# Performance work log

Measured on AMD Instinct MI355X. Metric: run time of the kernel, lower is better.

The kernel has to match this reference:

```python
import jax, jax.numpy as jnp
import numpy as np

HIDDEN = 1024
INTER = 4096
NUM_EXPERTS = 8
TOP_K = 2
NUM_TOKENS = 8192


def setup_inputs() -> dict:
    key = jax.random.key(0)
    k_x, k_r, k_w1, k_w2 = jax.random.split(key, 4)
    x = jax.random.normal(k_x, (NUM_TOKENS, HIDDEN), dtype=jnp.float32)
    router_w = jax.random.normal(k_r, (NUM_EXPERTS, HIDDEN), dtype=jnp.float32) * 0.02
    expert_w1 = jax.random.normal(k_w1, (NUM_EXPERTS, HIDDEN, INTER), dtype=jnp.float32) * 0.02
    # torch init: std = 0.02 / sqrt(2 * num_experts)
    expert_w2 = jax.random.normal(k_w2, (NUM_EXPERTS, INTER, HIDDEN), dtype=jnp.float32) * (0.02 / (2 * NUM_EXPERTS) ** 0.5)
    return {"x": x, "router_w": router_w, "expert_w1": expert_w1, "expert_w2": expert_w2}


def reference(x, router_w, expert_w1, expert_w2):
    num_tokens = x.shape[0]
    # Router: logits -> softmax -> top-k -> renormalize (matches torch.topk on probs)
    router_logits = x @ router_w.T                      # [T, E]
    probs = jax.nn.softmax(router_logits, axis=-1)       # [T, E]
    top_vals, top_idx = jax.lax.top_k(probs, TOP_K)      # [T, K]
    top_vals = top_vals / jnp.sum(top_vals, axis=-1, keepdims=True)

    # Auxiliary load-balancing loss (uses only the top-1 expert, as in torch code)
    expert_mask = jax.nn.one_hot(top_idx[:, 0], NUM_EXPERTS, dtype=x.dtype)  # [T, E]
    tokens_per_expert = expert_mask.sum(axis=0)                              # [E]
    router_prob = probs.mean(axis=0)                                         # [E]
    aux_loss = jnp.sum(tokens_per_expert / num_tokens * router_prob) * NUM_EXPERTS

    # Per-token combine weight for each expert (scatter top-k weights to dense [T, E])
    combine = jnp.zeros((num_tokens, NUM_EXPERTS), dtype=x.dtype)
    combine = combine.at[jnp.arange(num_tokens)[:, None], top_idx].add(top_vals)

    # Per-expert 2-layer MLP (silu), weighted combine. Loop over fixed small E.
    output = jnp.zeros_like(x)
    for e in range(NUM_EXPERTS):
        h = jax.nn.silu(x @ expert_w1[e])            # [T, I]
        output = output + combine[:, e:e + 1] * (h @ expert_w2[e])
    return output, aux_loss
```

## Files before the change

### kernel.cpp

```cpp
#include <hip/hip_runtime.h>
#include <hip/hip_bf16.h>
#include <stdint.h>

#define NTOK  8192
#define HID   1024
#define INTER 4096
#define NEXP  8
#define NSLOT (NTOK * 2)

typedef __attribute__((ext_vector_type(4))) float f32x4;
typedef __attribute__((ext_vector_type(8))) short bf16x8;
typedef __attribute__((ext_vector_type(4))) short bf16x4;

__device__ __forceinline__ short f2bf(float f) {
  union { float f; uint32_t u; } v; v.f = f;
  uint32_t u = v.u;
  u += 0x7FFFu + ((u >> 16) & 1u);
  return (short)(u >> 16);
}

__device__ __forceinline__ void glds16(const short* g, short* l) {
  __builtin_amdgcn_global_load_lds(
      (const __attribute__((address_space(1))) void*)g,
      (__attribute__((address_space(3))) void*)l, 16, 0, 0);
}

__global__ __launch_bounds__(256) void castx_k(const float* __restrict__ in,
                                               short* __restrict__ out) {
  size_t i = ((size_t)blockIdx.x * 256 + threadIdx.x) * 4;
  f32x4 v = *(const f32x4*)(in + i);
  bf16x4 o = { f2bf(v.x), f2bf(v.y), f2bf(v.z), f2bf(v.w) };
  *(bf16x4*)(out + i) = o;
}

__global__ __launch_bounds__(256) void router_k(
    const float* __restrict__ x, const float* __restrict__ rw,
    int* __restrict__ top_idx, float* __restrict__ top_w,
    float* __restrict__ probsum, float* __restrict__ cnt1) {
  __shared__ float lrw[NEXP * HID];
  __shared__ float red[4][2 * NEXP];
  int tid = threadIdx.x;
  for (int i = tid * 4; i < NEXP * HID; i += 1024)
    *(f32x4*)(lrw + i) = *(const f32x4*)(rw + i);
  __syncthreads();
  int lane = tid & 63;
  int wv = tid >> 6;
  float pacc[NEXP], cacc[NEXP];
#pragma unroll
  for (int e = 0; e < NEXP; e++) { pacc[e] = 0.f; cacc[e] = 0.f; }
#pragma unroll
  for (int it = 0; it < 4; it++) {
    int t = blockIdx.x * 16 + it * 4 + wv;
    const float* xr = x + (size_t)t * HID;
    float acc[NEXP];
#pragma unroll
    for (int e = 0; e < NEXP; e++) acc[e] = 0.f;
#pragma unroll
    for (int k4 = 0; k4 < 4; k4++) {
      int k = k4 * 256 + lane * 4;
      f32x4 xv = *(const f32x4*)(xr + k);
#pragma unroll
      for (int e = 0; e < NEXP; e++) {
        f32x4 rv = *(const f32x4*)(lrw + e * HID + k);
        acc[e] += xv.x * rv.x + xv.y * rv.y + xv.z * rv.z + xv.w * rv.w;
      }
    }
#pragma unroll
    for (int e = 0; e < NEXP; e++) {
#pragma unroll
      for (int off = 32; off > 0; off >>= 1)
        acc[e] += __shfl_xor(acc[e], off);
    }
    float mx = acc[0];
#pragma unroll
    for (int e = 1; e < NEXP; e++) mx = fmaxf(mx, acc[e]);
    float p[NEXP], s = 0.f;
#pragma unroll
    for (int e = 0; e < NEXP; e++) { p[e] = expf(acc[e] - mx); s += p[e]; }
    float inv = 1.f / s;
    float p1 = -1.f, p2 = -1.f; int i1 = 0, i2 = 0;
#pragma unroll
    for (int e = 0; e < NEXP; e++) {
      float pe = p[e] * inv;
      p[e] = pe;
      if (pe > p1)      { p2 = p1; i2 = i1; p1 = pe; i1 = e; }
      else if (pe > p2) { p2 = pe; i2 = e; }
    }
    if (lane == 0) {
      float rs = 1.f / (p1 + p2);
      top_idx[t * 2] = i1; top_idx[t * 2 + 1] = i2;
      top_w[t * 2] = p1 * rs; top_w[t * 2 + 1] = p2 * rs;
#pragma unroll
      for (int e = 0; e < NEXP; e++) {
        pacc[e] += p[e];
        cacc[e] += (i1 == e) ? 1.f : 0.f;
      }
    }
  }
  if (lane == 0) {
#pragma unroll
    for (int e = 0; e < NEXP; e++) {
      red[wv][e] = pacc[e];
      red[wv][NEXP + e] = cacc[e];
    }
  }
  __syncthreads();
  if (tid < NEXP) {
    float s = 0.f, c = 0.f;
#pragma unroll
    for (int w = 0; w < 4; w++) { s += red[w][tid]; c += red[w][NEXP + tid]; }
    atomicAdd(&probsum[tid], s);
    atomicAdd(&cnt1[tid], c);
  }
}

__global__ void aux_k(const float* probsum, const float* cnt1, float* out_aux) {
  if (threadIdx.x == 0 && blockIdx.x == 0) {
    float s = 0.f;
    for (int e = 0; e < NEXP; e++) s += cnt1[e] * probsum[e];
    out_aux[0] = s * (float)NEXP / ((float)NTOK * (float)NTOK);
  }
}

__global__ void lists_k(const int* __restrict__ top_idx, int* __restrict__ cnt,
                        int* __restrict__ lists) {
  int i = blockIdx.x * 256 + threadIdx.x;
  if (i < NSLOT) {
    int e = top_idx[i];
    int pos = atomicAdd(cnt + e, 1);
    lists[e * NTOK + pos] = i;
  }
}

__global__ __launch_bounds__(256) void transpose_k(
    const float* __restrict__ in, short* __restrict__ out, int K, int N) {
  __shared__ short tile[64][72];
  int e = blockIdx.z;
  in  += (size_t)e * K * N;
  out += (size_t)e * K * N;
  int n0 = blockIdx.x * 64, k0 = blockIdx.y * 64;
  int tid = threadIdx.x;
#pragma unroll
  for (int i = 0; i < 4; i++) {
    int k = (tid >> 4) + i * 16;
    int c = (tid & 15) * 4;
    f32x4 v = *(const f32x4*)(in + (size_t)(k0 + k) * N + n0 + c);
    tile[k][c] = f2bf(v.x); tile[k][c + 1] = f2bf(v.y);
    tile[k][c + 2] = f2bf(v.z); tile[k][c + 3] = f2bf(v.w);
  }
  __syncthreads();
#pragma unroll
  for (int i = 0; i < 2; i++) {
    int cid = tid + i * 256;
    int n = cid >> 3, kk = (cid & 7) * 8;
    bf16x8 o;
#pragma unroll
    for (int j = 0; j < 8; j++) o[j] = tile[kk + j][n];
    *(bf16x8*)(out + (size_t)(n0 + n) * K + k0 + kk) = o;
  }
}

template <int KDIM, bool L1>
__global__ __launch_bounds__(256) void moe_gemm_k(
    const short* __restrict__ A, const short* __restrict__ Bt,
    void* __restrict__ outp, const int* __restrict__ cnt,
    const int* __restrict__ lists, const float* __restrict__ top_w, int Ndim) {
  int e = blockIdx.z;
  int ce = cnt[e];
  int m0 = blockIdx.y * 128;
  if (m0 >= ce) return;
  int n0 = blockIdx.x * 128;
  const int* list = lists + e * NTOK;
  const short* B = Bt + (size_t)e * Ndim * KDIM;

  __shared__ short As[128 * 32];
  __shared__ short Bs[128 * 32];
  __shared__ int   sSlot[128];
  __shared__ float sW[128];

  int tid = threadIdx.x;
  if (tid < 128) {
    int idx = m0 + tid;
    if (idx >= ce) idx = ce - 1;
    int slot = list[idx];
    sSlot[tid] = slot;
    sW[tid] = L1 ? 0.f : top_w[slot];
  }
  __syncthreads();

  int r1 = tid >> 2, cs = tid & 3;
  int r2 = r1 + 64;
  int q1 = (cs ^ ((r1 >> 1) & 3)) * 8;
  int q2 = (cs ^ ((r2 >> 1) & 3)) * 8;
  int ar1 = L1 ? (sSlot[r1] >> 1) : sSlot[r1];
  int ar2 = L1 ? (sSlot[r2] >> 1) : sSlot[r2];
  const short* gA1 = A + (size_t)ar1 * KDIM + q1;
  const short* gA2 = A + (size_t)ar2 * KDIM + q2;
  const short* gB1 = B + (size_t)(n0 + r1) * KDIM + q1;
  const short* gB2 = B + (size_t)(n0 + r2) * KDIM + q2;
  short* lA1 = As + tid * 8;
  short* lA2 = As + 2048 + tid * 8;
  short* lB1 = Bs + tid * 8;
  short* lB2 = Bs + 2048 + tid * 8;

  int lane = tid & 63, wave = tid >> 6;
  int wm = wave & 1, wn = wave >> 1;
  int lr = lane & 15, quad = lane >> 4;
  int aoff[4], boff[4];
#pragma unroll
  for (int mi = 0; mi < 4; mi++) {
    int r = wm * 64 + mi * 16 + lr;
    aoff[mi] = r * 32 + (quad ^ ((r >> 1) & 3)) * 8;
  }
#pragma unroll
  for (int ni = 0; ni < 4; ni++) {
    int n = wn * 64 + ni * 16 + lr;
    boff[ni] = n * 32 + (quad ^ ((n >> 1) & 3)) * 8;
  }

  f32x4 acc[4][4] = {};

  for (int kt = 0; kt < KDIM / 32; kt++) {
    int ko = kt * 32;
    glds16(gA1 + ko, lA1);
    glds16(gA2 + ko, lA2);
    glds16(gB1 + ko, lB1);
    glds16(gB2 + ko, lB2);
    __syncthreads();
    bf16x8 af[4], bfg[4];
#pragma unroll
    for (int mi = 0; mi < 4; mi++) af[mi] = *(const bf16x8*)(As + aoff[mi]);
#pragma unroll
    for (int ni = 0; ni < 4; ni++) bfg[ni] = *(const bf16x8*)(Bs + boff[ni]);
#pragma unroll
    for (int mi = 0; mi < 4; mi++)
#pragma unroll
      for (int ni = 0; ni < 4; ni++)
        acc[mi][ni] = __builtin_amdgcn_mfma_f32_16x16x32_bf16(af[mi], bfg[ni], acc[mi][ni], 0, 0, 0);
    __syncthreads();
  }

  int ncol0 = n0 + wn * 64 + lr;
#pragma unroll
  for (int mi = 0; mi < 4; mi++) {
#pragma unroll
    for (int rg = 0; rg < 4; rg++) {
      int r = wm * 64 + mi * 16 + quad * 4 + rg;
      int gm = m0 + r;
      if (gm < ce) {
        int slot = sSlot[r];
#pragma unroll
        for (int ni = 0; ni < 4; ni++) {
          float v = acc[mi][ni][rg];
          int col = ncol0 + ni * 16;
          if (L1) {
            float sv = v / (1.f + expf(-v));
            ((short*)outp)[(size_t)slot * Ndim + col] = f2bf(sv);
          } else {
            atomicAdd((float*)outp + (size_t)(slot >> 1) * Ndim + col, v * sW[r]);
          }
        }
      }
    }
  }
}

extern "C" void kernel_launch(void* const* d_in, const int* in_sizes, int n_in,
                              void* d_out, int out_size, void* d_ws, size_t ws_size,
                              hipStream_t stream) {
  const float* x  = (const float*)d_in[0];
  const float* rw = (const float*)d_in[1];
  const float* w1 = (const float*)d_in[2];
  const float* w2 = (const float*)d_in[3];
  float* out = (float*)d_out;

  char* ws = (char*)d_ws;
  size_t off = 0;
  auto alloc = [&](size_t b) { void* p = ws + off; off += (b + 255) & ~(size_t)255; return p; };
  short* wt    = (short*)alloc((size_t)NEXP * HID * INTER * 2);
  short* h     = (short*)alloc((size_t)NSLOT * INTER * 2);
  short* xb    = (short*)alloc((size_t)NTOK * HID * 2);
  int*   tidx  = (int*)alloc(NSLOT * 4);
  float* tw    = (float*)alloc(NSLOT * 4);
  int*   lists = (int*)alloc(NEXP * NTOK * 4);
  int*   cnt   = (int*)alloc(256);
  float* probsum = (float*)(cnt + 8);
  float* cnt1    = (float*)(cnt + 16);

  hipMemsetAsync(cnt, 0, 256, stream);
  hipMemsetAsync(out, 0, (size_t)out_size * 4, stream);

  castx_k<<<(NTOK * HID / 4) / 256, 256, 0, stream>>>(x, xb);
  router_k<<<NTOK / 16, 256, 0, stream>>>(x, rw, tidx, tw, probsum, cnt1);
  aux_k<<<1, 64, 0, stream>>>(probsum, cnt1, out + (size_t)NTOK * HID);
  lists_k<<<NSLOT / 256, 256, 0, stream>>>(tidx, cnt, lists);

  transpose_k<<<dim3(INTER / 64, HID / 64, NEXP), 256, 0, stream>>>(w1, wt, HID, INTER);
  moe_gemm_k<HID, true><<<dim3(INTER / 128, NTOK / 128, NEXP), 256, 0, stream>>>(
      xb, wt, h, cnt, lists, tw, INTER);

  transpose_k<<<dim3(HID / 64, INTER / 64, NEXP), 256, 0, stream>>>(w2, wt, INTER, HID);
  moe_gemm_k<INTER, false><<<dim3(HID / 128, NTOK / 128, NEXP), 256, 0, stream>>>(
      h, wt, out, cnt, lists, tw, HID);
}
```

Before: 870.3 us.

## Double-buffer LDS tiles in MoE GEMM and remap workgroups across XCDs

The MoE expert GEMM now uses two LDS buffers, so the async global-to-LDS loads for the next K tile are issued while MFMAs run on the current one, removing one barrier stall per iteration. The 3D grid becomes a flattened 1D grid with an (id&7)*(NWG/8) remap, which places neighbouring tiles on the same XCD for L2 reuse of weights and A rows. N is now a template constant. LDS use doubles, which may reduce occupancy.

```diff
diff --git a/kernel.cpp b/kernel.cpp
--- a/kernel.cpp
+++ b/kernel.cpp
@@ -160,21 +160,30 @@
   }
 }
 
-template <int KDIM, bool L1>
+template <int KDIM, int NDIM, bool L1>
 __global__ __launch_bounds__(256) void moe_gemm_k(
     const short* __restrict__ A, const short* __restrict__ Bt,
     void* __restrict__ outp, const int* __restrict__ cnt,
-    const int* __restrict__ lists, const float* __restrict__ top_w, int Ndim) {
-  int e = blockIdx.z;
+    const int* __restrict__ lists, const float* __restrict__ top_w) {
+  constexpr int NB = NDIM / 128;
+  constexpr int MB = NTOK / 128;
+  constexpr int NWG = NB * MB * NEXP;
+  int id = blockIdx.x;
+  id = (id & 7) * (NWG >> 3) + (id >> 3);
+  int n = id % NB;
+  int rem = id / NB;
+  int m = rem % MB;
+  int e = rem / MB;
+
   int ce = cnt[e];
-  int m0 = blockIdx.y * 128;
+  int m0 = m * 128;
   if (m0 >= ce) return;
-  int n0 = blockIdx.x * 128;
+  int n0 = n * 128;
   const int* list = lists + e * NTOK;
-  const short* B = Bt + (size_t)e * Ndim * KDIM;
-
-  __shared__ short As[128 * 32];
-  __shared__ short Bs[128 * 32];
+  const short* B = Bt + (size_t)e * (size_t)NDIM * KDIM;
+
+  __shared__ short As[2][128 * 32];
+  __shared__ short Bs[2][128 * 32];
   __shared__ int   sSlot[128];
   __shared__ float sW[128];
 
@@ -198,10 +207,6 @@
   const short* gA2 = A + (size_t)ar2 * KDIM + q2;
   const short* gB1 = B + (size_t)(n0 + r1) * KDIM + q1;
   const short* gB2 = B + (size_t)(n0 + r2) * KDIM + q2;
-  short* lA1 = As + tid * 8;
-  short* lA2 = As + 2048 + tid * 8;
-  short* lB1 = Bs + tid * 8;
-  short* lB2 = Bs + 2048 + tid * 8;
 
   int lane = tid & 63, wave = tid >> 6;
   int wm = wave & 1, wn = wave >> 1;
@@ -214,31 +219,47 @@
   }
 #pragma unroll
   for (int ni = 0; ni < 4; ni++) {
-    int n = wn * 64 + ni * 16 + lr;
-    boff[ni] = n * 32 + (quad ^ ((n >> 1) & 3)) * 8;
+    int nn = wn * 64 + ni * 16 + lr;
+    boff[ni] = nn * 32 + (quad ^ ((nn >> 1) & 3)) * 8;
   }
 
   f32x4 acc[4][4] = {};
 
-  for (int kt = 0; kt < KDIM / 32; kt++) {
-    int ko = kt * 32;
-    glds16(gA1 + ko, lA1);
-    glds16(gA2 + ko, lA2);
-    glds16(gB1 + ko, lB1);
-    glds16(gB2 + ko, lB2);
+#define STAGE(buf, ko)                                  \
+  do {                                                  \
+    glds16(gA1 + (ko), As[buf] + tid * 8);              \
+    glds16(gA2 + (ko), As[buf] + 2048 + tid * 8);       \
+    glds16(gB1 + (ko), Bs[buf] + tid * 8);              \
+    glds16(gB2 + (ko), Bs[buf] + 2048 + tid * 8);       \
+  } while (0)
+
+#define COMPUTE(buf)                                                          \
+  do {                                                                        \
+    bf16x8 af[4], bfg[4];                                                     \
+    _Pragma("unroll")                                                         \
+    for (int mi = 0; mi < 4; mi++) af[mi] = *(const bf16x8*)(As[buf] + aoff[mi]); \
+    _Pragma("unroll")                                                         \
+    for (int ni = 0; ni < 4; ni++) bfg[ni] = *(const bf16x8*)(Bs[buf] + boff[ni]); \
+    _Pragma("unroll")                                                         \
+    for (int mi = 0; mi < 4; mi++)                                            \
+      _Pragma("unroll")                                                       \
+      for (int ni = 0; ni < 4; ni++)                                          \
+        acc[mi][ni] = __builtin_amdgcn_mfma_f32_16x16x32_bf16(af[mi], bfg[ni], acc[mi][ni], 0, 0, 0); \
+  } while (0)
+
+  constexpr int NK = KDIM / 32;
+  STAGE(0, 0);
+  __syncthreads();
+  for (int kt = 0; kt < NK; kt += 2) {
+    STAGE(1, (kt + 1) * 32);
+    COMPUTE(0);
     __syncthreads();
-    bf16x8 af[4], bfg[4];
-#pragma unroll
-    for (int mi = 0; mi < 4; mi++) af[mi] = *(const bf16x8*)(As + aoff[mi]);
-#pragma unroll
-    for (int ni = 0; ni < 4; ni++) bfg[ni] = *(const bf16x8*)(Bs + boff[ni]);
-#pragma unroll
-    for (int mi = 0; mi < 4; mi++)
-#pragma unroll
-      for (int ni = 0; ni < 4; ni++)
-        acc[mi][ni] = __builtin_amdgcn_mfma_f32_16x16x32_bf16(af[mi], bfg[ni], acc[mi][ni], 0, 0, 0);
+    if (kt + 2 < NK) STAGE(0, (kt + 2) * 32);
+    COMPUTE(1);
     __syncthreads();
   }
+#undef STAGE
+#undef COMPUTE
 
   int ncol0 = n0 + wn * 64 + lr;
 #pragma unroll
@@ -255,9 +276,9 @@
           int col = ncol0 + ni * 16;
           if (L1) {
             float sv = v / (1.f + expf(-v));
-            ((short*)outp)[(size_t)slot * Ndim + col] = f2bf(sv);
+            ((short*)outp)[(size_t)slot * NDIM + col] = f2bf(sv);
           } else {
-            atomicAdd((float*)outp + (size_t)(slot >> 1) * Ndim + col, v * sW[r]);
+            atomicAdd((float*)outp + (size_t)(slot >> 1) * NDIM + col, v * sW[r]);
           }
         }
       }
@@ -296,10 +317,12 @@
   lists_k<<<NSLOT / 256, 256, 0, stream>>>(tidx, cnt, lists);
 
   transpose_k<<<dim3(INTER / 64, HID / 64, NEXP), 256, 0, stream>>>(w1, wt, HID, INTER);
-  moe_gemm_k<HID, true><<<dim3(INTER / 128, NTOK / 128, NEXP), 256, 0, stream>>>(
-      xb, wt, h, cnt, lists, tw, INTER);
+  moe_gemm_k<HID, INTER, true>
+      <<<(INTER / 128) * (NTOK / 128) * NEXP, 256, 0, stream>>>(
+          xb, wt, h, cnt, lists, tw);
 
   transpose_k<<<dim3(HID / 64, INTER / 64, NEXP), 256, 0, stream>>>(w2, wt, INTER, HID);
-  moe_gemm_k<INTER, false><<<dim3(HID / 128, NTOK / 128, NEXP), 256, 0, stream>>>(
-      h, wt, out, cnt, lists, tw, HID);
-}
+  moe_gemm_k<INTER, HID, false>
+      <<<(HID / 128) * (NTOK / 128) * NEXP, 256, 0, stream>>>(
+          h, wt, out, cnt, lists, tw);
+}
```

Measured after the change: 869.9 us. About the same (-0.0%).
